# Kernel optimization log

Hardware: AMD Instinct MI355X
Metric: run time of the kernel (lower is better)

## Reference

```python
import jax, jax.numpy as jnp
import numpy as np

N_QUBITS = 16
N_LAYERS = 6
BATCH = 512


def _apply_1q(state, U, q, n, batched):
    """Apply a single-qubit gate U to qubit q of state (B, 2**n).
    U: (2,2) shared, or (B,2,2) per-sample if batched."""
    B = state.shape[0]
    d0, d1 = 2 ** q, 2 ** (n - q - 1)
    s = state.reshape(B, d0, 2, d1)
    if batched:
        s = jnp.einsum('bij,bxjy->bxiy', U, s)
    else:
        s = jnp.einsum('ij,bxjy->bxiy', U, s)
    return s.reshape(B, -1)


def _apply_cnot(state, c, t, n):
    """CNOT with control c, target t on state (B, 2**n)."""
    B = state.shape[0]
    a, b = (c, t) if c < t else (t, c)
    d0, d1, d2 = 2 ** a, 2 ** (b - a - 1), 2 ** (n - b - 1)
    s = state.reshape(B, d0, 2, d1, 2, d2)
    if c < t:  # control = axis 2, target = axis 4: flip target where control==1
        s = jnp.concatenate([s[:, :, :1], jnp.flip(s[:, :, 1:], axis=4)], axis=2)
    else:      # control = axis 4, target = axis 2
        s = jnp.concatenate([s[:, :, :, :, :1], jnp.flip(s[:, :, :, :, 1:], axis=2)], axis=4)
    return s.reshape(B, -1)


def _rx(theta):
    """RX(theta) for a batch of angles -> (B,2,2) complex64."""
    c = jnp.cos(theta * 0.5).astype(jnp.complex64)
    s = (-1j * jnp.sin(theta * 0.5)).astype(jnp.complex64)
    return jnp.stack([jnp.stack([c, s], -1), jnp.stack([s, c], -1)], -2)


def _rot(phi, theta, omega):
    """PennyLane Rot(phi,theta,omega) = RZ(omega) RY(theta) RZ(phi) -> (2,2) complex64."""
    c = jnp.cos(theta * 0.5)
    s = jnp.sin(theta * 0.5)
    m00 = jnp.exp(-0.5j * (phi + omega)) * c
    m01 = -jnp.exp(0.5j * (phi - omega)) * s
    m10 = jnp.exp(-0.5j * (phi - omega)) * s
    m11 = jnp.exp(0.5j * (phi + omega)) * c
    return jnp.stack([jnp.stack([m00, m01]), jnp.stack([m10, m11])]).astype(jnp.complex64)


def _circuit(x, weights, n, n_layers):
    B = x.shape[0]
    state = jnp.zeros((B, 2 ** n), dtype=jnp.complex64).at[:, 0].set(1.0)
    # AngleEmbedding: default rotation is RX(x_q) on wire q (per-sample angles)
    for q in range(n):
        state = _apply_1q(state, _rx(x[:, q]), q, n, batched=True)
    # StronglyEntanglingLayers: Rot on each wire, then ring of CNOTs with range r
    for l in range(n_layers):
        for q in range(n):
            U = _rot(weights[l, q, 0], weights[l, q, 1], weights[l, q, 2])
            state = _apply_1q(state, U, q, n, batched=False)
        r = (l % (n - 1)) + 1  # PennyLane default ranges
        for q in range(n):
            state = _apply_cnot(state, q, (q + r) % n, n)
    # <Z_q> = P(bit_q = 0) - P(bit_q = 1)
    probs = state.real ** 2 + state.imag ** 2  # (B, 2**n)
    exps = []
    for q in range(n):
        p = probs.reshape(B, 2 ** q, 2, -1).sum(axis=(1, 3))  # (B, 2)
        exps.append(p[:, 0] - p[:, 1])
    return jnp.stack(exps, axis=-1)  # (B, n)


def setup_inputs() -> dict:
    key = jax.random.key(0)
    kx, kw = jax.random.split(key)
    x = jax.random.normal(kx, (BATCH, N_QUBITS), dtype=jnp.float32)
    weights = jax.random.normal(kw, (N_LAYERS, N_QUBITS, 3), dtype=jnp.float32)
    return {"x": x, "weights": weights}


def reference(x, weights):
    return _circuit(x, weights, N_QUBITS, N_LAYERS)
```

## Files before the change

kernel.cpp:

```cpp
#include <hip/hip_runtime.h>


#define NTH 512
typedef float v32f __attribute__((ext_vector_type(32)));

template <int I> struct IC { static constexpr int value = I; };
template <int N, int I = 0, typename F>
__device__ __forceinline__ void static_for(F&& f) {
  if constexpr (I < N) { f(IC<I>{}); static_for<N, I + 1>(f); }
}


template <int LB>
__device__ __forceinline__ void rot_local(v32f& ar, v32f& ai, const float* __restrict__ u) {
  const float u00r = u[0], u00i = u[1], u01r = u[2], u01i = u[3];
  const float u10r = u[4], u10i = u[5], u11r = u[6], u11i = u[7];
  static_for<16>([&](auto hc) {
    constexpr int h = hc.value;
    constexpr int e0 = ((h >> LB) << (LB + 1)) | (h & ((1 << LB) - 1));
    constexpr int e1 = e0 | (1 << LB);
    const float axr = ar[e0], axi = ai[e0], bxr = ar[e1], bxi = ai[e1];
    ar[e0] = u00r * axr - u00i * axi + u01r * bxr - u01i * bxi;
    ai[e0] = u00r * axi + u00i * axr + u01r * bxi + u01i * bxr;
    ar[e1] = u10r * axr - u10i * axi + u11r * bxr - u11i * bxi;
    ai[e1] = u10r * axi + u10i * axr + u11r * bxi + u11i * bxr;
  });
}

__device__ __forceinline__ void rot_lane(v32f& ar, v32f& ai, const float* __restrict__ u,
                                         const int m, const int bit) {
  const float car = bit ? u[6] : u[0], cai = bit ? u[7] : u[1];
  const float cbr = bit ? u[4] : u[2], cbi = bit ? u[5] : u[3];
  static_for<32>([&](auto ec) {
    constexpr int e = ec.value;
    const float orr = ar[e], oii = ai[e];
    const float pr = __shfl_xor(orr, m);
    const float pi = __shfl_xor(oii, m);
    ar[e] = car * orr - cai * oii + cbr * pr - cbi * pi;
    ai[e] = car * oii + cai * orr + cbr * pi + cbi * pr;
  });
}

template <int TB, int LOCALLO, int C>
__device__ __forceinline__ void cnot_local(v32f& ar, v32f& ai, const int ibase) {
  static_for<16>([&](auto hc) {
    constexpr int h = hc.value;
    constexpr int e0 = ((h >> TB) << (TB + 1)) | (h & ((1 << TB) - 1));
    constexpr int e1 = e0 | (1 << TB);
    if constexpr (C >= LOCALLO && C < LOCALLO + 5) {
      if constexpr ((e0 >> (C - LOCALLO)) & 1) {
        const float tr = ar[e0], ti = ai[e0];
        ar[e0] = ar[e1]; ai[e0] = ai[e1];
        ar[e1] = tr;     ai[e1] = ti;
      }
    } else {
      const int take = (ibase >> C) & 1;
      const float axr = ar[e0], axi = ai[e0], bxr = ar[e1], bxi = ai[e1];
      ar[e0] = take ? bxr : axr; ai[e0] = take ? bxi : axi;
      ar[e1] = take ? axr : bxr; ai[e1] = take ? axi : bxi;
    }
  });
}

template <int LOCALLO, int C>
__device__ __forceinline__ void cnot_lane(v32f& ar, v32f& ai, const int m, const int ibase) {
  if constexpr (C >= LOCALLO && C < LOCALLO + 5) {
    static_for<32>([&](auto ec) {
      constexpr int e = ec.value;
      if constexpr ((e >> (C - LOCALLO)) & 1) {
        ar[e] = __shfl_xor(ar[e], m);
        ai[e] = __shfl_xor(ai[e], m);
      }
    });
  } else {
    const int take = (ibase >> C) & 1;
    static_for<32>([&](auto ec) {
      constexpr int e = ec.value;
      const float pr = __shfl_xor(ar[e], m);
      const float pi = __shfl_xor(ai[e], m);
      ar[e] = take ? pr : ar[e];
      ai[e] = take ? pi : ai[e];
    });
  }
}

__global__ void qsim_prep(const float* __restrict__ w, float* __restrict__ gm) {
  const int i = threadIdx.x;
  if (i < 96) {
    const float phi = w[i * 3 + 0];
    const float th  = w[i * 3 + 1];
    const float om  = w[i * 3 + 2];
    float st, ct; sincosf(0.5f * th, &st, &ct);
    float sa, ca; sincosf(0.5f * (phi + om), &sa, &ca);
    float sb, cb; sincosf(0.5f * (phi - om), &sb, &cb);
    float* u = gm + i * 8;
    u[0] =  ct * ca; u[1] = -ct * sa;
    u[2] = -st * cb; u[3] = -st * sb;
    u[4] =  st * cb; u[5] = -st * sb;
    u[6] =  ct * ca; u[7] =  ct * sa;
  }
}

template <int L>
__global__ void __launch_bounds__(NTH) sweepP(float2* __restrict__ st,
                                              const float* __restrict__ x,
                                              const float* __restrict__ gm) {
  const int tid = threadIdx.x;
  const int s  = blockIdx.x >> 2;
  const int fb = blockIdx.x & 3;
  const int ibase = (((tid >> 3) & 7) << 5) | (((tid >> 6) & 7) << 8) |
                    (fb << 11) | ((tid & 7) << 13);
  const int pbase = ((tid >> 3) & 7) | ((tid & 7) << 3) |
                    (((tid >> 6) & 7) << 11) | (fb << 14);
  float2* __restrict__ base = st + (s << 16) + pbase;
  constexpr int r = L + 1;
  const float* __restrict__ gl = gm + L * 128;
  v32f ar, ai;

  if constexpr (L == 0) {
    __shared__ float iv[16][4];
    if (tid < 16) {
      const float* u = gm + tid * 8;
      float sx, cx; sincosf(0.5f * x[s * 16 + tid], &sx, &cx);
      iv[tid][0] = u[0] * cx + u[3] * sx;
      iv[tid][1] = u[1] * cx - u[2] * sx;
      iv[tid][2] = u[4] * cx + u[7] * sx;
      iv[tid][3] = u[5] * cx - u[6] * sx;
    }
    __syncthreads();
    float Tr = 1.f, Ti = 0.f;
    #pragma unroll
    for (int b = 5; b <= 15; ++b) {
      const int bit = (ibase >> b) & 1;
      const float fr = iv[b][2 * bit], fi = iv[b][2 * bit + 1];
      const float nr = Tr * fr - Ti * fi; Ti = Tr * fi + Ti * fr; Tr = nr;
    }
    ar[0] = Tr; ai[0] = Ti;
    static_for<5>([&](auto bc) {
      constexpr int bI = bc.value;
      const float v0r = iv[bI][0], v0i = iv[bI][1], v1r = iv[bI][2], v1i = iv[bI][3];
      static_for<(1 << bI)>([&](auto kc) {
        constexpr int k = kc.value;
        constexpr int k1 = k | (1 << bI);
        const float kr = ar[k], ki = ai[k];
        ar[k1] = kr * v1r - ki * v1i; ai[k1] = kr * v1i + ki * v1r;
        ar[k]  = kr * v0r - ki * v0i; ai[k]  = kr * v0i + ki * v0r;
      });
    });
  } else {
    #pragma unroll
    for (int e = 0; e < 32; ++e) {
      const float2 v = base[e << 6];
      ar[e] = v.x; ai[e] = v.y;
    }
    static_for<L>([&](auto kc) {
      constexpr int k = kc.value;
      constexpr int C = 16 - L + k;
      cnot_local<k, 0, C>(ar, ai, ibase);
    });
    rot_local<0>(ar, ai, gl);
    rot_local<1>(ar, ai, gl + 8);
    rot_local<2>(ar, ai, gl + 16);
    rot_local<3>(ar, ai, gl + 24);
    rot_local<4>(ar, ai, gl + 32);
    rot_lane(ar, ai, gl + 40, 8,  (tid >> 3) & 1);
    rot_lane(ar, ai, gl + 48, 16, (tid >> 4) & 1);
    rot_lane(ar, ai, gl + 56, 32, (tid >> 5) & 1);
  }

  static_for<8 - r>([&](auto gc) {
    constexpr int g = gc.value;
    constexpr int t = g + r;
    if constexpr (t <= 4) cnot_local<t, 0, g>(ar, ai, ibase);
    else                  cnot_lane<0, g>(ar, ai, 1 << (t - 2), ibase);
  });

  #pragma unroll
  for (int e = 0; e < 32; ++e) {
    float2 v; v.x = ar[e]; v.y = ai[e];
    base[e << 6] = v;
  }
}

template <int L>
__global__ void __launch_bounds__(NTH) sweepQ(float2* __restrict__ st,
                                              const float* __restrict__ gm) {
  const int tid = threadIdx.x;
  const int s  = blockIdx.x >> 2;
  const int fb = blockIdx.x & 3;
  const int ibase = ((tid >> 6) & 7) | (fb << 3) | ((tid & 7) << 5) |
                    (((tid >> 3) & 7) << 13);
  const int pbase = (tid & 7) | (((tid >> 3) & 7) << 3) |
                    (((tid >> 6) & 7) << 6) | (fb << 9);
  float2* __restrict__ base = st + (s << 16) + pbase;
  constexpr int r = L + 1;
  const float* __restrict__ gl = gm + L * 128;
  v32f ar, ai;
  #pragma unroll
  for (int e = 0; e < 32; ++e) {
    const float2 v = base[e << 11];
    ar[e] = v.x; ai[e] = v.y;
  }
  if constexpr (L > 0) {
    rot_local<0>(ar, ai, gl + 64);
    rot_local<1>(ar, ai, gl + 72);
    rot_local<2>(ar, ai, gl + 80);
    rot_local<3>(ar, ai, gl + 88);
    rot_local<4>(ar, ai, gl + 96);
    rot_lane(ar, ai, gl + 104, 8,  (tid >> 3) & 1);
    rot_lane(ar, ai, gl + 112, 16, (tid >> 4) & 1);
    rot_lane(ar, ai, gl + 120, 32, (tid >> 5) & 1);
  }
  static_for<8>([&](auto gc) {
    constexpr int g = 8 - r + gc.value;
    constexpr int t = g + r;
    if constexpr (t <= 12) cnot_local<t - 8, 8, g>(ar, ai, ibase);
    else                   cnot_lane<8, g>(ar, ai, 1 << (t - 10), ibase);
  });

  #pragma unroll
  for (int e = 0; e < 32; ++e) {
    float2 v; v.x = ar[e]; v.y = ai[e];
    base[e << 11] = v;
  }
}

__global__ void __launch_bounds__(NTH) finalK(const float2* __restrict__ st,
                                              float* __restrict__ part) {
  const int tid = threadIdx.x;
  const int s  = blockIdx.x >> 2;
  const int fb = blockIdx.x & 3;
  const int ibase = (((tid >> 3) & 7) << 5) | (((tid >> 6) & 7) << 8) |
                    (fb << 11) | ((tid & 7) << 13);
  const int pbase = ((tid >> 3) & 7) | ((tid & 7) << 3) |
                    (((tid >> 6) & 7) << 11) | (fb << 14);
  const float2* __restrict__ base = st + (s << 16) + pbase;
  v32f ar, ai;
  #pragma unroll
  for (int e = 0; e < 32; ++e) {
    const float2 v = base[e << 6];
    ar[e] = v.x; ai[e] = v.y;
  }
  static_for<6>([&](auto kc) {
    constexpr int k = kc.value;
    constexpr int C = 10 + k;
    if constexpr (k <= 4) cnot_local<k, 0, C>(ar, ai, ibase);
    else                  cnot_lane<0, C>(ar, ai, 8, ibase);
  });
  __shared__ float red[8][16];
  float tot = 0.f, sl0 = 0.f, sl1 = 0.f, sl2 = 0.f, sl3 = 0.f, sl4 = 0.f;
  static_for<32>([&](auto ec) {
    constexpr int e = ec.value;
    const float p = ar[e] * ar[e] + ai[e] * ai[e];
    tot += p;
    if constexpr (e & 1)  sl0 -= p; else sl0 += p;
    if constexpr (e & 2)  sl1 -= p; else sl1 += p;
    if constexpr (e & 4)  sl2 -= p; else sl2 += p;
    if constexpr (e & 8)  sl3 -= p; else sl3 += p;
    if constexpr (e & 16) sl4 -= p; else sl4 += p;
  });
  const float sl[5] = {sl0, sl1, sl2, sl3, sl4};
  const int wv = tid >> 6;
  static_for<16>([&](auto qc) {
    constexpr int q = qc.value;
    float v;
    if constexpr (q < 5) v = sl[q];
    else v = ((ibase >> q) & 1) ? -tot : tot;
    v += __shfl_xor(v, 1);  v += __shfl_xor(v, 2);  v += __shfl_xor(v, 4);
    v += __shfl_xor(v, 8);  v += __shfl_xor(v, 16); v += __shfl_xor(v, 32);
    if ((tid & 63) == 0) red[wv][q] = v;
  });
  __syncthreads();
  if (tid < 16) {
    float a = 0.f;
    #pragma unroll
    for (int w8 = 0; w8 < 8; ++w8) a += red[w8][tid];
    part[blockIdx.x * 16 + tid] = a;
  }
}

__global__ void __launch_bounds__(NTH) reduceK(const float* __restrict__ part,
                                               float* __restrict__ out) {
  const int j = blockIdx.x * NTH + threadIdx.x;
  const int s = j >> 4, q = j & 15;
  float a = 0.f;
  #pragma unroll
  for (int f = 0; f < 4; ++f) a += part[(s << 6) + f * 16 + q];
  out[j] = a;
}

extern "C" void kernel_launch(void* const* d_in, const int* in_sizes, int n_in,
                              void* d_out, int out_size, void* d_ws, size_t ws_size,
                              hipStream_t stream) {
  (void)in_sizes; (void)n_in; (void)out_size;
  const float* x = (const float*)d_in[0];
  const float* w = (const float*)d_in[1];
  float* out = (float*)d_out;
  float* gm   = (float*)d_ws;
  float* part = (float*)((char*)d_ws + 4096);
  float2* st  = (float2*)((char*)d_ws + 524288);

  const size_t avail = ws_size > 524288 ? ws_size - 524288 : 0;
  long long chunk = (long long)(avail / 524288);
  if (chunk > 256) chunk = 256;
  if (chunk < 1) chunk = 1;

  qsim_prep<<<dim3(1), dim3(128), 0, stream>>>(w, gm);
  for (int s0 = 0; s0 < 512; s0 += (int)chunk) {
    const int ns = (512 - s0) < (int)chunk ? (512 - s0) : (int)chunk;
    const dim3 g(ns * 4), b(NTH);
    const float* xs = x + s0 * 16;
    float* pp = part + (size_t)s0 * 64;
    sweepP<0><<<g, b, 0, stream>>>(st, xs, gm);
    sweepQ<0><<<g, b, 0, stream>>>(st, gm);
    sweepP<1><<<g, b, 0, stream>>>(st, xs, gm);
    sweepQ<1><<<g, b, 0, stream>>>(st, gm);
    sweepP<2><<<g, b, 0, stream>>>(st, xs, gm);
    sweepQ<2><<<g, b, 0, stream>>>(st, gm);
    sweepP<3><<<g, b, 0, stream>>>(st, xs, gm);
    sweepQ<3><<<g, b, 0, stream>>>(st, gm);
    sweepP<4><<<g, b, 0, stream>>>(st, xs, gm);
    sweepQ<4><<<g, b, 0, stream>>>(st, gm);
    sweepP<5><<<g, b, 0, stream>>>(st, xs, gm);
    sweepQ<5><<<g, b, 0, stream>>>(st, gm);
    finalK<<<g, b, 0, stream>>>(st, pp);
  }
  reduceK<<<dim3(16), dim3(NTH), 0, stream>>>(part, out);
}
```

Measured before the change: 1.714 ms.

## Ping-pong state buffers with transposed layouts between P and Q sweeps

```diff
diff --git a/kernel.cpp b/kernel.cpp
--- a/kernel.cpp
+++ b/kernel.cpp
@@ -102,7 +102,8 @@
 }
 
 template <int L>
-__global__ void __launch_bounds__(NTH) sweepP(float2* __restrict__ st,
+__global__ void __launch_bounds__(NTH) sweepP(const float2* __restrict__ sin,
+                                              float2* __restrict__ sout,
                                               const float* __restrict__ x,
                                               const float* __restrict__ gm) {
   const int tid = threadIdx.x;
@@ -110,9 +111,12 @@
   const int fb = blockIdx.x & 3;
   const int ibase = (((tid >> 3) & 7) << 5) | (((tid >> 6) & 7) << 8) |
                     (fb << 11) | ((tid & 7) << 13);
-  const int pbase = ((tid >> 3) & 7) | ((tid & 7) << 3) |
-                    (((tid >> 6) & 7) << 11) | (fb << 14);
-  float2* __restrict__ base = st + (s << 16) + pbase;
+  const int rpb = ((tid >> 3) & 7) | ((tid & 7) << 3) |
+                  (((tid >> 6) & 7) << 6) | (fb << 9);
+  const int wpb = ((tid >> 3) & 7) | ((tid & 7) << 3) |
+                  (((tid >> 6) & 7) << 11) | (fb << 14);
+  const float2* __restrict__ rbase = sin + (s << 16) + rpb;
+  float2* __restrict__ wbase = sout + (s << 16) + wpb;
   constexpr int r = L + 1;
   const float* __restrict__ gl = gm + L * 128;
   v32f ar, ai;
@@ -150,7 +154,7 @@
   } else {
     #pragma unroll
     for (int e = 0; e < 32; ++e) {
-      const float2 v = base[e << 6];
+      const float2 v = rbase[e << 11];
       ar[e] = v.x; ai[e] = v.y;
     }
     static_for<L>([&](auto kc) {
@@ -178,27 +182,31 @@
   #pragma unroll
   for (int e = 0; e < 32; ++e) {
     float2 v; v.x = ar[e]; v.y = ai[e];
-    base[e << 6] = v;
+    wbase[e << 6] = v;
   }
 }
 
 template <int L>
-__global__ void __launch_bounds__(NTH) sweepQ(float2* __restrict__ st,
+__global__ void __launch_bounds__(NTH) sweepQ(const float2* __restrict__ sin,
+                                              float2* __restrict__ sout,
                                               const float* __restrict__ gm) {
   const int tid = threadIdx.x;
   const int s  = blockIdx.x >> 2;
   const int fb = blockIdx.x & 3;
   const int ibase = ((tid >> 6) & 7) | (fb << 3) | ((tid & 7) << 5) |
                     (((tid >> 3) & 7) << 13);
-  const int pbase = (tid & 7) | (((tid >> 3) & 7) << 3) |
-                    (((tid >> 6) & 7) << 6) | (fb << 9);
-  float2* __restrict__ base = st + (s << 16) + pbase;
+  const int rpb = (tid & 7) | (((tid >> 3) & 7) << 3) |
+                  (((tid >> 6) & 7) << 6) | (fb << 9);
+  const int wpb = (tid & 7) | (((tid >> 3) & 7) << 3) |
+                  (((tid >> 6) & 7) << 11) | (fb << 14);
+  const float2* __restrict__ rbase = sin + (s << 16) + rpb;
+  float2* __restrict__ wbase = sout + (s << 16) + wpb;
   constexpr int r = L + 1;
   const float* __restrict__ gl = gm + L * 128;
   v32f ar, ai;
   #pragma unroll
   for (int e = 0; e < 32; ++e) {
-    const float2 v = base[e << 11];
+    const float2 v = rbase[e << 11];
     ar[e] = v.x; ai[e] = v.y;
   }
   if constexpr (L > 0) {
@@ -221,24 +229,24 @@
   #pragma unroll
   for (int e = 0; e < 32; ++e) {
     float2 v; v.x = ar[e]; v.y = ai[e];
-    base[e << 11] = v;
-  }
-}
-
-__global__ void __launch_bounds__(NTH) finalK(const float2* __restrict__ st,
+    wbase[e << 6] = v;
+  }
+}
+
+__global__ void __launch_bounds__(NTH) finalK(const float2* __restrict__ sin,
                                               float* __restrict__ part) {
   const int tid = threadIdx.x;
   const int s  = blockIdx.x >> 2;
   const int fb = blockIdx.x & 3;
   const int ibase = (((tid >> 3) & 7) << 5) | (((tid >> 6) & 7) << 8) |
                     (fb << 11) | ((tid & 7) << 13);
-  const int pbase = ((tid >> 3) & 7) | ((tid & 7) << 3) |
-                    (((tid >> 6) & 7) << 11) | (fb << 14);
-  const float2* __restrict__ base = st + (s << 16) + pbase;
+  const int rpb = ((tid >> 3) & 7) | ((tid & 7) << 3) |
+                  (((tid >> 6) & 7) << 6) | (fb << 9);
+  const float2* __restrict__ rbase = sin + (s << 16) + rpb;
   v32f ar, ai;
   #pragma unroll
   for (int e = 0; e < 32; ++e) {
-    const float2 v = base[e << 6];
+    const float2 v = rbase[e << 11];
     ar[e] = v.x; ai[e] = v.y;
   }
   static_for<6>([&](auto kc) {
@@ -298,12 +306,12 @@
   float* out = (float*)d_out;
   float* gm   = (float*)d_ws;
   float* part = (float*)((char*)d_ws + 4096);
-  float2* st  = (float2*)((char*)d_ws + 524288);
-
   const size_t avail = ws_size > 524288 ? ws_size - 524288 : 0;
-  long long chunk = (long long)(avail / 524288);
-  if (chunk > 256) chunk = 256;
+  long long chunk = (long long)(avail / 1048576);
+  if (chunk > 128) chunk = 128;
   if (chunk < 1) chunk = 1;
+  float2* st0 = (float2*)((char*)d_ws + 524288);
+  float2* st1 = (float2*)((char*)d_ws + 524288 + (size_t)chunk * 524288);
 
   qsim_prep<<<dim3(1), dim3(128), 0, stream>>>(w, gm);
   for (int s0 = 0; s0 < 512; s0 += (int)chunk) {
@@ -311,19 +319,19 @@
     const dim3 g(ns * 4), b(NTH);
     const float* xs = x + s0 * 16;
     float* pp = part + (size_t)s0 * 64;
-    sweepP<0><<<g, b, 0, stream>>>(st, xs, gm);
-    sweepQ<0><<<g, b, 0, stream>>>(st, gm);
-    sweepP<1><<<g, b, 0, stream>>>(st, xs, gm);
-    sweepQ<1><<<g, b, 0, stream>>>(st, gm);
-    sweepP<2><<<g, b, 0, stream>>>(st, xs, gm);
-    sweepQ<2><<<g, b, 0, stream>>>(st, gm);
-    sweepP<3><<<g, b, 0, stream>>>(st, xs, gm);
-    sweepQ<3><<<g, b, 0, stream>>>(st, gm);
-    sweepP<4><<<g, b, 0, stream>>>(st, xs, gm);
-    sweepQ<4><<<g, b, 0, stream>>>(st, gm);
-    sweepP<5><<<g, b, 0, stream>>>(st, xs, gm);
-    sweepQ<5><<<g, b, 0, stream>>>(st, gm);
-    finalK<<<g, b, 0, stream>>>(st, pp);
+    sweepP<0><<<g, b, 0, stream>>>(st1, st0, xs, gm);
+    sweepQ<0><<<g, b, 0, stream>>>(st0, st1, gm);
+    sweepP<1><<<g, b, 0, stream>>>(st1, st0, xs, gm);
+    sweepQ<1><<<g, b, 0, stream>>>(st0, st1, gm);
+    sweepP<2><<<g, b, 0, stream>>>(st1, st0, xs, gm);
+    sweepQ<2><<<g, b, 0, stream>>>(st0, st1, gm);
+    sweepP<3><<<g, b, 0, stream>>>(st1, st0, xs, gm);
+    sweepQ<3><<<g, b, 0, stream>>>(st0, st1, gm);
+    sweepP<4><<<g, b, 0, stream>>>(st1, st0, xs, gm);
+    sweepQ<4><<<g, b, 0, stream>>>(st0, st1, gm);
+    sweepP<5><<<g, b, 0, stream>>>(st1, st0, xs, gm);
+    sweepQ<5><<<g, b, 0, stream>>>(st0, st1, gm);
+    finalK<<<g, b, 0, stream>>>(st1, pp);
   }
   reduceK<<<dim3(16), dim3(NTH), 0, stream>>>(part, out);
 }
```

Result: slower. 2.631 ms (+53.5%).
